# Performance work log

Hardware: AMD Instinct MI355X
Metric: run time of the kernel (lower is better)

Reference implementation:

```python
import jax, jax.numpy as jnp
import numpy as np

TEMPERATURE = 0.1
EPS = 1e-8  # matches torch F.cosine_similarity norm clamp

N, D = 4096, 256

def setup_inputs() -> dict:
    key = jax.random.key(0)
    k1, k2 = jax.random.split(key)
    z_i = jax.random.normal(k1, (N, D), dtype=jnp.float32)
    z_j = jax.random.normal(k2, (N, D), dtype=jnp.float32)
    return {"z_i": z_i, "z_j": z_j}

def reference(z_i, z_j):
    n = z_i.shape[0]
    z = jnp.concatenate([z_i, z_j], axis=0)              # [2N, D]
    # cosine similarity via normalized Gram matrix (faithful to F.cosine_similarity)
    norms = jnp.maximum(jnp.linalg.norm(z, axis=-1, keepdims=True), EPS)
    zn = z / norms                                        # [2N, D]
    sim = (zn @ zn.T) / TEMPERATURE                       # [2N, 2N]
    # mask self-similarity on the diagonal
    diag = jnp.eye(2 * n, dtype=bool)
    sim = jnp.where(diag, -jnp.inf, sim)
    # labels: positive of i is i+N (and vice versa)
    labels = jnp.concatenate([jnp.arange(n, 2 * n), jnp.arange(0, n)])
    logp = jax.nn.log_softmax(sim, axis=-1)               # [2N, 2N]
    nll = -jnp.take_along_axis(logp, labels[:, None], axis=-1)[:, 0]
    return jnp.mean(nll)
```

## Files before the change

kernel.cpp:

```cpp
#include <hip/hip_runtime.h>
#include <hip/hip_bf16.h>

#define NHALF 4096
#define TWO_N 8192
#define DDIM 256
#define INV_T 10.0f
#define SCALE 14.426950408889634f
#define KBSTRIDE ((size_t)TWO_N * 64)

typedef __bf16 v8bf __attribute__((ext_vector_type(8)));
typedef float f32x4 __attribute__((ext_vector_type(4)));

#if __has_builtin(__builtin_amdgcn_exp2f)
#define EXP2F(x) __builtin_amdgcn_exp2f(x)
#else
#define EXP2F(x) exp2f(x)
#endif

static __device__ __forceinline__ unsigned int f2bf(float x) {
    __hip_bfloat16 h = __float2bfloat16(x);
    return (unsigned int)*(unsigned short*)&h;
}

__global__ __launch_bounds__(256) void ntx_norm_kernel(
    const float* __restrict__ zi, const float* __restrict__ zj,
    char* __restrict__ znB, float* __restrict__ rowacc,
    float* __restrict__ out) {
    const int w = threadIdx.x >> 6;
    const int lane = threadIdx.x & 63;
    const int r = blockIdx.x * 4 + w;
    const float* src = (r < NHALF) ? (zi + (size_t)r * DDIM)
                                   : (zj + (size_t)(r - NHALF) * DDIM);
    float4 v = ((const float4*)src)[lane];
    float ss = v.x * v.x + v.y * v.y + v.z * v.z + v.w * v.w;
#pragma unroll
    for (int m = 1; m < 64; m <<= 1) ss += __shfl_xor(ss, m);
    float rinv = 1.0f / fmaxf(sqrtf(ss), 1e-8f);
    uint2 pk;
    pk.x = f2bf(v.x * rinv) | (f2bf(v.y * rinv) << 16);
    pk.y = f2bf(v.z * rinv) | (f2bf(v.w * rinv) << 16);
    char* dst = znB + (size_t)(lane >> 3) * KBSTRIDE + (size_t)r * 64 +
                ((lane >> 1) & 3) * 16 + (lane & 1) * 8;
    *(uint2*)dst = pk;
    if (blockIdx.x < 32) rowacc[blockIdx.x * 256 + threadIdx.x] = 0.0f;
    if (blockIdx.x == 0 && threadIdx.x == 0) out[0] = 0.0f;
}

__global__ __launch_bounds__(256, 2) void ntx_gram_kernel(
    const char* __restrict__ znB,
    float* __restrict__ rowacc,
    float* __restrict__ spos) {
    const int tid = threadIdx.x;
    const int w = tid >> 6, lane = tid & 63;
    const int task = blockIdx.x * 4 + w;
    const int lrow = lane & 15, lk = lane >> 4;

    bool odg[4];
#pragma unroll
    for (int j = 0; j < 4; ++j) odg[j] = (lrow == lk * 4 + j);

    f32x4 af[4][8];
    float rowsum[4][4];
    int rbase;

#define LOAD_AF()                                                             \
    do {                                                                      \
        _Pragma("unroll")                                                     \
        for (int rf = 0; rf < 4; ++rf) {                                      \
            const char* ab =                                                  \
                znB + (size_t)(rbase + rf * 16 + lrow) * 64 + lk * 16;        \
            _Pragma("unroll")                                                 \
            for (int kb = 0; kb < 8; ++kb)                                    \
                af[rf][kb] = *(const f32x4*)(ab + kb * KBSTRIDE);             \
        }                                                                     \
        _Pragma("unroll")                                                     \
        for (int rf = 0; rf < 4; ++rf)                                        \
            _Pragma("unroll")                                                 \
            for (int kb = 0; kb < 8; ++kb)                                    \
                asm volatile("" : "+v"(af[rf][kb]));  \
    } while (0)

#define ZERO_RS()                                                             \
    do {                                                                      \
        _Pragma("unroll")                                                     \
        for (int rf = 0; rf < 4; ++rf)                                        \
            _Pragma("unroll")                                                 \
            for (int j = 0; j < 4; ++j) rowsum[rf][j] = 0.0f;                 \
    } while (0)

#define LOADB(bf, cf)                                                         \
    do {                                                                      \
        _Pragma("unroll")                                                     \
        for (int kb = 0; kb < 8; ++kb)                                        \
            bf[kb] = *(const f32x4*)(zcb + (cf) * 1024 + kb * KBSTRIDE);      \
    } while (0)

#define COMPUTE_EPI(bf, cf)                                                   \
    do {                                                                      \
        f32x4 acc[4];                                                         \
        _Pragma("unroll")                                                     \
        for (int rf = 0; rf < 4; ++rf) acc[rf] = (f32x4){0.f, 0.f, 0.f, 0.f}; \
        _Pragma("unroll")                                                     \
        for (int kb = 0; kb < 8; ++kb) {                                      \
            _Pragma("unroll")                                                 \
            for (int rf = 0; rf < 4; ++rf)                                    \
                acc[rf] = __builtin_amdgcn_mfma_f32_16x16x32_bf16(            \
                    __builtin_bit_cast(v8bf, af[rf][kb]),                     \
                    __builtin_bit_cast(v8bf, bf[kb]), acc[rf], 0, 0, 0);      \
        }                                                                     \
        float ce = 0.0f;                                                      \
        _Pragma("unroll")                                                     \
        for (int rf = 0; rf < 4; ++rf) {                                      \
            const bool dfrag = (rf == (cf));                                  \
            _Pragma("unroll")                                                 \
            for (int j = 0; j < 4; ++j) {                                     \
                const float sv = acc[rf][j];                                  \
                const bool od = dfrag && odg[j];                              \
                if (posb && od) {                                             \
                    const int u = rf * 16 + lk * 4 + j;                       \
                    spos[rbase + u] = sv * INV_T;                             \
                    spos[cb + u] = sv * INV_T;                                \
                }                                                             \
                float e = EXP2F(sv * SCALE);                                  \
                e = (self && od) ? 0.0f : e;                                  \
                rowsum[rf][j] += e;                                           \
                ce += e;                                                      \
            }                                                                 \
        }                                                                     \
        if (!self) {                                                          \
            ce += __shfl_xor(ce, 16);                                         \
            ce += __shfl_xor(ce, 32);                                         \
            if (lane < 16)                                                    \
                atomicAdd(&rowacc[cb + (cf) * 16 + lrow], ce);                \
        }                                                                     \
    } while (0)

#define DO_TILE(dd, SELF, POSB)                                               \
    do {                                                                      \
        const int ct = (((rbase >> 6) - (dd)) + 128) & 127;                   \
        const int cb = ct * 64;                                               \
        const bool self = (SELF);                                             \
        const bool posb = (POSB);                                             \
        const char* zcb = znB + (size_t)(cb + lrow) * 64 + lk * 16;           \
        f32x4 bfA[8], bfB[8];                                                 \
        LOADB(bfA, 0);                                                        \
        LOADB(bfB, 1);                                                        \
        COMPUTE_EPI(bfA, 0);                                                  \
        LOADB(bfA, 2);                                                        \
        COMPUTE_EPI(bfB, 1);                                                  \
        LOADB(bfB, 3);                                                        \
        COMPUTE_EPI(bfA, 2);                                                  \
        COMPUTE_EPI(bfB, 3);                                                  \
    } while (0)

#define FLUSH_RS()                                                            \
    do {                                                                      \
        _Pragma("unroll")                                                     \
        for (int rf = 0; rf < 4; ++rf) {                                      \
            _Pragma("unroll")                                                 \
            for (int j = 0; j < 4; ++j) {                                     \
                float v = rowsum[rf][j];                                      \
                v += __shfl_xor(v, 1);                                        \
                v += __shfl_xor(v, 2);                                        \
                v += __shfl_xor(v, 4);                                        \
                v += __shfl_xor(v, 8);                                        \
                if (lrow == 0)                                                \
                    atomicAdd(&rowacc[rbase + rf * 16 + lk * 4 + j], v);      \
            }                                                                 \
        }                                                                     \
    } while (0)

    if (task < 16) {
#pragma unroll 1
        for (int s = 0; s < 4; ++s) {
            rbase = (task * 4 + s) * 64;
            LOAD_AF();
            ZERO_RS();
            DO_TILE(64, false, true);
            FLUSH_RS();
        }
    } else {
        const int t = task - 16;
        const int rt = t >> 4, g = t & 15;
        rbase = rt * 64;
        LOAD_AF();
        ZERO_RS();
#pragma unroll 1
        for (int s = 0; s < 4; ++s) {
            const int d = g * 4 + s;
            DO_TILE(d, d == 0, false);
        }
        FLUSH_RS();
    }
#undef LOAD_AF
#undef ZERO_RS
#undef LOADB
#undef COMPUTE_EPI
#undef DO_TILE
#undef FLUSH_RS
}

__global__ __launch_bounds__(256) void ntx_final_kernel(
    const float* __restrict__ rowacc, const float* __restrict__ spos,
    float* __restrict__ out) {
    const int tid = threadIdx.x;
    const int r = blockIdx.x * 256 + tid;
    float nll = logf(rowacc[r]) - spos[r];
    __shared__ float red[256];
    red[tid] = nll;
    __syncthreads();
    for (int s = 128; s > 0; s >>= 1) {
        if (tid < s) red[tid] += red[tid + s];
        __syncthreads();
    }
    if (tid == 0) atomicAdd(out, red[0] * (1.0f / (float)TWO_N));
}

extern "C" void kernel_launch(void* const* d_in, const int* in_sizes, int n_in,
                              void* d_out, int out_size, void* d_ws, size_t ws_size,
                              hipStream_t stream) {
    const float* zi = (const float*)d_in[0];
    const float* zj = (const float*)d_in[1];
    char* ws = (char*)d_ws;
    char* znB = ws;
    size_t off = (size_t)TWO_N * DDIM * 2;
    float* spos = (float*)(ws + off);
    off += (size_t)TWO_N * 4;
    float* rowacc = (float*)(ws + off);
    float* out = (float*)d_out;

    ntx_norm_kernel<<<TWO_N / 4, 256, 0, stream>>>(zi, zj, znB, rowacc, out);
    ntx_gram_kernel<<<516, 256, 0, stream>>>(znB, rowacc, spos);
    ntx_final_kernel<<<TWO_N / 256, 256, 0, stream>>>(rowacc, spos, out);
}
```

Before: 54.49 us.

## Halve per-wave row tile to 32 rows and double waves for higher occupancy

Each wave now keeps a 32-row A fragment instead of 64 rows, and the B fragments are loaded in two half-K chunks of 4 rather than double-buffered full 8-chunk fragments. This cuts VGPR usage so launch bounds can request 4 blocks per SM, and the grid doubles to 1032 blocks. The aim is more waves in flight to hide global-load latency. In exchange, each B tile is loaded twice as often relative to the compute, there is less in-wave prefetch overlap, and there are more column atomics.

```diff
diff --git a/kernel.cpp b/kernel.cpp
--- a/kernel.cpp
+++ b/kernel.cpp
@@ -46,7 +46,7 @@
     if (blockIdx.x == 0 && threadIdx.x == 0) out[0] = 0.0f;
 }
 
-__global__ __launch_bounds__(256, 2) void ntx_gram_kernel(
+__global__ __launch_bounds__(256, 4) void ntx_gram_kernel(
     const char* __restrict__ znB,
     float* __restrict__ rowacc,
     float* __restrict__ spos) {
@@ -55,26 +55,22 @@
     const int task = blockIdx.x * 4 + w;
     const int lrow = lane & 15, lk = lane >> 4;
 
-    bool odg[4];
-#pragma unroll
-    for (int j = 0; j < 4; ++j) odg[j] = (lrow == lk * 4 + j);
-
-    f32x4 af[4][8];
-    float rowsum[4][4];
-    int rbase;
+    f32x4 af[2][8], bf[4];
+    float rowsum[2][4];
+    int R0, halfv;
 
 #define LOAD_AF()                                                             \
     do {                                                                      \
         _Pragma("unroll")                                                     \
-        for (int rf = 0; rf < 4; ++rf) {                                      \
+        for (int rf = 0; rf < 2; ++rf) {                                      \
             const char* ab =                                                  \
-                znB + (size_t)(rbase + rf * 16 + lrow) * 64 + lk * 16;        \
+                znB + (size_t)(R0 + rf * 16 + lrow) * 64 + lk * 16;           \
             _Pragma("unroll")                                                 \
             for (int kb = 0; kb < 8; ++kb)                                    \
                 af[rf][kb] = *(const f32x4*)(ab + kb * KBSTRIDE);             \
         }                                                                     \
         _Pragma("unroll")                                                     \
-        for (int rf = 0; rf < 4; ++rf)                                        \
+        for (int rf = 0; rf < 2; ++rf)                                        \
             _Pragma("unroll")                                                 \
             for (int kb = 0; kb < 8; ++kb)                                    \
                 asm volatile("" : "+v"(af[rf][kb]));  \
@@ -83,80 +79,81 @@
 #define ZERO_RS()                                                             \
     do {                                                                      \
         _Pragma("unroll")                                                     \
-        for (int rf = 0; rf < 4; ++rf)                                        \
+        for (int rf = 0; rf < 2; ++rf)                                        \
             _Pragma("unroll")                                                 \
             for (int j = 0; j < 4; ++j) rowsum[rf][j] = 0.0f;                 \
     } while (0)
 
-#define LOADB(bf, cf)                                                         \
-    do {                                                                      \
-        _Pragma("unroll")                                                     \
-        for (int kb = 0; kb < 8; ++kb)                                        \
+#define CFSTEP(cf, C0, SELF, POSB)                                            \
+    do {                                                                      \
+        f32x4 acc[2];                                                         \
+        acc[0] = (f32x4){0.f, 0.f, 0.f, 0.f};                                 \
+        acc[1] = (f32x4){0.f, 0.f, 0.f, 0.f};                                 \
+        _Pragma("unroll")                                                     \
+        for (int kb = 0; kb < 4; ++kb)                                        \
             bf[kb] = *(const f32x4*)(zcb + (cf) * 1024 + kb * KBSTRIDE);      \
-    } while (0)
-
-#define COMPUTE_EPI(bf, cf)                                                   \
-    do {                                                                      \
-        f32x4 acc[4];                                                         \
-        _Pragma("unroll")                                                     \
-        for (int rf = 0; rf < 4; ++rf) acc[rf] = (f32x4){0.f, 0.f, 0.f, 0.f}; \
-        _Pragma("unroll")                                                     \
-        for (int kb = 0; kb < 8; ++kb) {                                      \
-            _Pragma("unroll")                                                 \
-            for (int rf = 0; rf < 4; ++rf)                                    \
-                acc[rf] = __builtin_amdgcn_mfma_f32_16x16x32_bf16(            \
-                    __builtin_bit_cast(v8bf, af[rf][kb]),                     \
-                    __builtin_bit_cast(v8bf, bf[kb]), acc[rf], 0, 0, 0);      \
+        _Pragma("unroll")                                                     \
+        for (int kb = 0; kb < 4; ++kb) {                                      \
+            acc[0] = __builtin_amdgcn_mfma_f32_16x16x32_bf16(                 \
+                __builtin_bit_cast(v8bf, af[0][kb]),                          \
+                __builtin_bit_cast(v8bf, bf[kb]), acc[0], 0, 0, 0);           \
+            acc[1] = __builtin_amdgcn_mfma_f32_16x16x32_bf16(                 \
+                __builtin_bit_cast(v8bf, af[1][kb]),                          \
+                __builtin_bit_cast(v8bf, bf[kb]), acc[1], 0, 0, 0);           \
+        }                                                                     \
+        _Pragma("unroll")                                                     \
+        for (int kb = 0; kb < 4; ++kb)                                        \
+            bf[kb] =                                                          \
+                *(const f32x4*)(zcb + (cf) * 1024 + (kb + 4) * KBSTRIDE);     \
+        _Pragma("unroll")                                                     \
+        for (int kb = 0; kb < 4; ++kb) {                                      \
+            acc[0] = __builtin_amdgcn_mfma_f32_16x16x32_bf16(                 \
+                __builtin_bit_cast(v8bf, af[0][kb + 4]),                      \
+                __builtin_bit_cast(v8bf, bf[kb]), acc[0], 0, 0, 0);           \
+            acc[1] = __builtin_amdgcn_mfma_f32_16x16x32_bf16(                 \
+                __builtin_bit_cast(v8bf, af[1][kb + 4]),                      \
+                __builtin_bit_cast(v8bf, bf[kb]), acc[1], 0, 0, 0);           \
         }                                                                     \
         float ce = 0.0f;                                                      \
         _Pragma("unroll")                                                     \
-        for (int rf = 0; rf < 4; ++rf) {                                      \
-            const bool dfrag = (rf == (cf));                                  \
+        for (int rf = 0; rf < 2; ++rf) {                                      \
+            const bool dfrag = ((cf) == halfv * 2 + rf);                      \
             _Pragma("unroll")                                                 \
             for (int j = 0; j < 4; ++j) {                                     \
                 const float sv = acc[rf][j];                                  \
-                const bool od = dfrag && odg[j];                              \
-                if (posb && od) {                                             \
-                    const int u = rf * 16 + lk * 4 + j;                       \
-                    spos[rbase + u] = sv * INV_T;                             \
-                    spos[cb + u] = sv * INV_T;                                \
+                const bool od = dfrag && (lrow == lk * 4 + j);                \
+                if ((POSB) && od) {                                           \
+                    const int u = R0 + rf * 16 + lk * 4 + j;                  \
+                    spos[u] = sv * INV_T;                                     \
+                    spos[u + NHALF] = sv * INV_T;                             \
                 }                                                             \
                 float e = EXP2F(sv * SCALE);                                  \
-                e = (self && od) ? 0.0f : e;                                  \
+                e = ((SELF) && od) ? 0.0f : e;                                \
                 rowsum[rf][j] += e;                                           \
                 ce += e;                                                      \
             }                                                                 \
         }                                                                     \
-        if (!self) {                                                          \
+        if (!(SELF)) {                                                        \
             ce += __shfl_xor(ce, 16);                                         \
             ce += __shfl_xor(ce, 32);                                         \
             if (lane < 16)                                                    \
-                atomicAdd(&rowacc[cb + (cf) * 16 + lrow], ce);                \
-        }                                                                     \
-    } while (0)
-
-#define DO_TILE(dd, SELF, POSB)                                               \
-    do {                                                                      \
-        const int ct = (((rbase >> 6) - (dd)) + 128) & 127;                   \
-        const int cb = ct * 64;                                               \
-        const bool self = (SELF);                                             \
-        const bool posb = (POSB);                                             \
-        const char* zcb = znB + (size_t)(cb + lrow) * 64 + lk * 16;           \
-        f32x4 bfA[8], bfB[8];                                                 \
-        LOADB(bfA, 0);                                                        \
-        LOADB(bfB, 1);                                                        \
-        COMPUTE_EPI(bfA, 0);                                                  \
-        LOADB(bfA, 2);                                                        \
-        COMPUTE_EPI(bfB, 1);                                                  \
-        LOADB(bfB, 3);                                                        \
-        COMPUTE_EPI(bfA, 2);                                                  \
-        COMPUTE_EPI(bfB, 3);                                                  \
+                atomicAdd(&rowacc[(C0) + (cf) * 16 + lrow], ce);              \
+        }                                                                     \
+    } while (0)
+
+#define DO_TILE(C0, SELF, POSB)                                               \
+    do {                                                                      \
+        const char* zcb = znB + (size_t)((C0) + lrow) * 64 + lk * 16;         \
+        CFSTEP(0, C0, SELF, POSB);                                            \
+        CFSTEP(1, C0, SELF, POSB);                                            \
+        CFSTEP(2, C0, SELF, POSB);                                            \
+        CFSTEP(3, C0, SELF, POSB);                                            \
     } while (0)
 
 #define FLUSH_RS()                                                            \
     do {                                                                      \
         _Pragma("unroll")                                                     \
-        for (int rf = 0; rf < 4; ++rf) {                                      \
+        for (int rf = 0; rf < 2; ++rf) {                                      \
             _Pragma("unroll")                                                 \
             for (int j = 0; j < 4; ++j) {                                     \
                 float v = rowsum[rf][j];                                      \
@@ -165,37 +162,46 @@
                 v += __shfl_xor(v, 4);                                        \
                 v += __shfl_xor(v, 8);                                        \
                 if (lrow == 0)                                                \
-                    atomicAdd(&rowacc[rbase + rf * 16 + lk * 4 + j], v);      \
+                    atomicAdd(&rowacc[R0 + rf * 16 + lk * 4 + j], v);         \
             }                                                                 \
         }                                                                     \
     } while (0)
 
-    if (task < 16) {
+    if (task < 32) {
 #pragma unroll 1
         for (int s = 0; s < 4; ++s) {
-            rbase = (task * 4 + s) * 64;
+            const int p = task * 4 + s;
+            R0 = p * 32;
+            halfv = p & 1;
+            const int C0 = (p >> 1) * 64 + NHALF;
             LOAD_AF();
             ZERO_RS();
-            DO_TILE(64, false, true);
+            DO_TILE(C0, false, true);
             FLUSH_RS();
         }
     } else {
-        const int t = task - 16;
-        const int rt = t >> 4, g = t & 15;
-        rbase = rt * 64;
+        const int t = task - 32;
+        const int rt128 = t >> 5, g = t & 15;
+        halfv = (t >> 4) & 1;
+        R0 = rt128 * 64 + halfv * 32;
         LOAD_AF();
         ZERO_RS();
 #pragma unroll 1
         for (int s = 0; s < 4; ++s) {
             const int d = g * 4 + s;
-            DO_TILE(d, d == 0, false);
+            const int ct = ((rt128 - d) + 128) & 127;
+            const int C0 = ct * 64;
+            if (d == 0) {
+                DO_TILE(C0, true, false);
+            } else {
+                DO_TILE(C0, false, false);
+            }
         }
         FLUSH_RS();
     }
 #undef LOAD_AF
 #undef ZERO_RS
-#undef LOADB
-#undef COMPUTE_EPI
+#undef CFSTEP
 #undef DO_TILE
 #undef FLUSH_RS
 }
@@ -230,6 +236,6 @@
     float* out = (float*)d_out;
 
     ntx_norm_kernel<<<TWO_N / 4, 256, 0, stream>>>(zi, zj, znB, rowacc, out);
-    ntx_gram_kernel<<<516, 256, 0, stream>>>(znB, rowacc, spos);
+    ntx_gram_kernel<<<1032, 256, 0, stream>>>(znB, rowacc, spos);
     ntx_final_kernel<<<TWO_N / 256, 256, 0, stream>>>(rowacc, spos, out);
 }
```

After: 72.12 us. 32.3% more time.
